# Kernel tuning notes

Hardware: AMD Instinct MI355X
Metric: run time of the kernel (lower is better)

Reference implementation:

```python
import jax, jax.numpy as jnp
import numpy as np

N = 50000   # n_nodes
F = 500     # n_features
D = 256     # architecture (GCN hidden)
K = 16      # n_clusters
E = 800000  # nnz of adjacency
CLUSTER_REG = 1.0
CON_REG = 0.5


def setup_inputs() -> dict:
    key = jax.random.key(0)
    ks = jax.random.split(key, 8)
    features = jax.random.normal(ks[0], (1, N, F), dtype=jnp.float32)
    aug_features = jax.random.normal(ks[1], (1, N, F), dtype=jnp.float32)
    graph_row = jax.random.randint(ks[2], (E,), 0, N, dtype=jnp.int32)
    graph_col = jax.random.randint(ks[3], (E,), 0, N, dtype=jnp.int32)
    graph_vals = jnp.ones((E,), jnp.float32)              # binary adjacency values
    gn_vals = jax.random.uniform(ks[4], (E,), jnp.float32)  # normalised adjacency values
    lbl = jnp.zeros((1, 2 * N), jnp.float32)              # unused in forward
    dense_graph = jnp.zeros((1,), jnp.float32)            # unused in forward
    # GCN params: Linear(F->D, bias=False) + separate zero bias (DGI-style GCN)
    W1 = jax.random.normal(ks[5], (D, F), dtype=jnp.float32) / np.sqrt(F)
    b1 = jnp.zeros((D,), jnp.float32)
    # transform: Linear(D->K) orthogonal-init weight, zero bias
    Wt = jax.random.normal(ks[6], (K, D), dtype=jnp.float32) / np.sqrt(D)
    bt = jnp.zeros((K,), jnp.float32)
    return {"features": features, "aug_features": aug_features,
            "graph_row": graph_row, "graph_col": graph_col,
            "graph_vals": graph_vals, "gn_vals": gn_vals,
            "lbl": lbl, "dense_graph": dense_graph,
            "W1": W1, "b1": b1, "Wt": Wt, "bt": bt}


def _spmm(row, col, vals, X):
    # (sparse NxN) @ X : out[i] = sum_j A[i,j] X[j]
    return jax.ops.segment_sum(vals[:, None] * X[col], row, num_segments=N)


def reference(features, aug_features, graph_row, graph_col, graph_vals, gn_vals,
              lbl, dense_graph, W1, b1, Wt, bt):
    def gcn(x):  # x: [1, N, F] -> [N, D]
        h = jnp.einsum('nf,df->nd', x[0], W1)      # Linear, no bias
        h = _spmm(graph_row, graph_col, gn_vals, h)  # A_norm @ h
        return jax.nn.selu(h + b1)

    gcn_out = gcn(features)                                  # [N, D]
    assignments = jax.nn.softmax(gcn_out @ Wt.T + bt, axis=1)  # [N, K]

    n_edges = jnp.float32(graph_vals.shape[0])
    degrees = jax.ops.segment_sum(graph_vals, graph_col, num_segments=N)[:, None]  # [N,1]

    AS = _spmm(graph_row, graph_col, graph_vals, assignments)  # A @ S, [N, K]
    graph_pooled = AS.T @ assignments                          # S^T A S, [K, K]
    nl = assignments.T @ degrees                               # [K, 1]
    normalizer = (nl @ nl.T) / 2.0 / n_edges                   # [K, K]
    spectral_loss = -jnp.trace(graph_pooled - normalizer) / 2.0 / n_edges

    cluster_sizes = assignments.sum(axis=0)                    # [K]
    cluster_loss = (jnp.linalg.norm(cluster_sizes) / N * np.sqrt(float(K)) - 1.0) * CLUSTER_REG

    aug_out = gcn(aug_features)                                # [N, D]
    # nn.CrossEntropyLoss(input=[1,N,D], target=[1,N,D] soft probs): class dim is N
    logsm = jax.nn.log_softmax(gcn_out, axis=0)                # softmax over nodes (dim=1 of [1,N,D])
    con_loss = -(aug_out * logsm).sum(axis=0).mean()

    return spectral_loss + cluster_loss + CON_REG * con_loss
```

## Files before the change

### kernel.cpp

```cpp
#include <hip/hip_runtime.h>
#include <math.h>

#define N_NODES 50000
#define N_FEAT  500
#define DH      256
#define KC      16
#define NE      800000
#define KPAD    512
#define MPAD    50048
#define M2      (2 * MPAD)
#define SLICE_COLS 32
#define NPAIR   8
#define SPMM_BLOCKS 2048
#define ROWS_PER_BLK 196
#define POST_BLOCKS 2048
#define SCAN_BLOCKS 196

#define R16(X) X(0) X(1) X(2) X(3) X(4) X(5) X(6) X(7) \
               X(8) X(9) X(10) X(11) X(12) X(13) X(14) X(15)

typedef __attribute__((ext_vector_type(8))) short short8;
typedef __attribute__((ext_vector_type(4))) float f32x4;

__device__ __forceinline__ unsigned short f2bf(float f) {
  unsigned u = __float_as_uint(f);
  u += 0x7FFFu + ((u >> 16) & 1u);
  return (unsigned short)(u >> 16);
}

__device__ __forceinline__ float bf2f(unsigned short u) {
  return __uint_as_float((unsigned)u << 16);
}

__device__ __forceinline__ float selu_f(float x) {
  return 1.0507009873554805f * (x > 0.f ? x : 1.6732632423543772f * expm1f(x));
}

__device__ __forceinline__ void gload16(const void* g, void* l) {
  __builtin_amdgcn_global_load_lds(
      (const __attribute__((address_space(1))) unsigned int*)g,
      (__attribute__((address_space(3))) unsigned int*)l, 16, 0, 0);
}

__global__ void k_cvt_w1(const float* __restrict__ in, unsigned short* __restrict__ out) {
  const int idx = blockIdx.x * 256 + threadIdx.x;
  if (idx >= DH * (KPAD / 8)) return;
  const int row = idx >> 6;
  const int cc  = idx & 63;
  const int scc = (cc & ~7) | ((cc & 7) ^ (row & 7));
  const int c0 = scc * 8;
  short8 w;
#pragma unroll
  for (int j = 0; j < 8; ++j) {
    const int col = c0 + j;
    w[j] = (col < N_FEAT) ? (short)f2bf(in[(size_t)row * N_FEAT + col]) : (short)0;
  }
  *(short8*)(out + (size_t)row * KPAD + cc * 8) = w;
}

__global__ __launch_bounds__(512, 2) void k_gemm_fused(
    const float* __restrict__ Af, const float* __restrict__ Aa,
    const unsigned short* __restrict__ Wbf, unsigned short* __restrict__ XWs) {
  __shared__ short As[128 * 64];
  __shared__ short Bs[256 * 64];
  const int t = threadIdx.x;
  const int lane = t & 63, wave = t >> 6;
  const int wr = (wave >> 2) * 64, wc = (wave & 3) * 64;
  const int bm = blockIdx.x * 128;
  const bool isaug = bm >= MPAD;
  const float* __restrict__ src = isaug ? Aa : Af;
  const int row0 = isaug ? bm - MPAD : bm;
  const int lr = lane & 15, lk = (lane >> 4) * 8;
  const int rsw = (lr & 7) * 8;
  const int ar = t >> 3, ac = (t & 7) * 8;
  const int aw = ac ^ ((ar & 7) * 8);
  f32x4 acc[4][4] = {};
  for (int kb = 0; kb < KPAD; kb += 64) {
    float4 ua[2][2];
#pragma unroll
    for (int h = 0; h < 2; ++h) {
      const int gr = row0 + ar + h * 64;
      const bool vr = gr < N_NODES;
      const float* arow = src + (size_t)(vr ? gr : 0) * N_FEAT;
      const int c = kb + ac;
      ua[h][0] = *(const float4*)(arow + min(c, N_FEAT - 4));
      ua[h][1] = *(const float4*)(arow + min(c + 4, N_FEAT - 4));
    }
#pragma unroll
    for (int i = 0; i < 4; ++i) {
      const int chunk = i * 512 + t;
      const int rb = chunk >> 3, sub = (chunk & 7) * 8;
      gload16(Wbf + (size_t)rb * KPAD + kb + sub, (void*)(Bs + (size_t)chunk * 8));
    }
#pragma unroll
    for (int h = 0; h < 2; ++h) {
      const int gr = row0 + ar + h * 64;
      const bool vr = gr < N_NODES;
      const int c = kb + ac;
      const bool ok0 = vr && (c < N_FEAT);
      const bool ok1 = vr && (c + 4 < N_FEAT);
      float4 u0 = ua[h][0], u1 = ua[h][1];
      u0.x = ok0 ? u0.x : 0.f; u0.y = ok0 ? u0.y : 0.f;
      u0.z = ok0 ? u0.z : 0.f; u0.w = ok0 ? u0.w : 0.f;
      u1.x = ok1 ? u1.x : 0.f; u1.y = ok1 ? u1.y : 0.f;
      u1.z = ok1 ? u1.z : 0.f; u1.w = ok1 ? u1.w : 0.f;
      short8 w;
      w[0] = (short)f2bf(u0.x); w[1] = (short)f2bf(u0.y);
      w[2] = (short)f2bf(u0.z); w[3] = (short)f2bf(u0.w);
      w[4] = (short)f2bf(u1.x); w[5] = (short)f2bf(u1.y);
      w[6] = (short)f2bf(u1.z); w[7] = (short)f2bf(u1.w);
      *(short8*)(As + (size_t)(ar + h * 64) * 64 + aw) = w;
    }
    __syncthreads();
#pragma unroll
    for (int kk = 0; kk < 64; kk += 32) {
      short8 af[4], bfr[4];
#pragma unroll
      for (int mi = 0; mi < 4; ++mi)
        af[mi] = *(const short8*)(As + (wr + mi * 16 + lr) * 64 + ((kk + lk) ^ rsw));
#pragma unroll
      for (int n = 0; n < 4; ++n)
        bfr[n] = *(const short8*)(Bs + (wc + n * 16 + lr) * 64 + ((kk + lk) ^ rsw));
#pragma unroll
      for (int mi = 0; mi < 4; ++mi)
#pragma unroll
        for (int n = 0; n < 4; ++n)
          acc[mi][n] = __builtin_amdgcn_mfma_f32_16x16x32_bf16(af[mi], bfr[n], acc[mi][n], 0, 0, 0);
    }
    __syncthreads();
  }
  const int crow = (lane >> 4) * 4, ccol = lane & 15;
  const int phb8 = isaug ? NPAIR : 0;
  const int snode = t >> 2, ssub = t & 3;
  const int csw = (snode & 7) * 8;
#pragma unroll
  for (int cb = 0; cb < 4; ++cb) {
    if ((wave & 3) == cb) {
#pragma unroll
      for (int mi = 0; mi < 4; ++mi)
#pragma unroll
        for (int n = 0; n < 4; ++n)
#pragma unroll
          for (int r = 0; r < 4; ++r)
            As[(wr + mi * 16 + crow + r) * 64 +
               ((n * 16 + ccol) ^ (((crow + r) & 7) * 8))] =
                (short)f2bf(acc[mi][n][r]);
    }
    __syncthreads();
#pragma unroll
    for (int p2 = 0; p2 < 2; ++p2) {
      const int pair = phb8 + cb * 2 + p2;
      const short8 vv = *(const short8*)(As + snode * 64 + ((p2 * 32 + ssub * 8) ^ csw));
      *(short8*)(XWs + ((size_t)pair * MPAD + row0 + snode) * SLICE_COLS + ssub * 8) = vv;
    }
    __syncthreads();
  }
}

__global__ void k_count(const int* __restrict__ row, int* __restrict__ counts) {
  const int e = blockIdx.x * blockDim.x + threadIdx.x;
  if (e < NE) atomicAdd(&counts[row[e]], 1);
}

__global__ __launch_bounds__(256) void k_scan_blk(const int* __restrict__ counts,
                                                  int* __restrict__ bsum) {
  __shared__ int red[256];
  const int t = threadIdx.x;
  const int j = blockIdx.x * 256 + t;
  red[t] = (j < N_NODES) ? counts[j] : 0;
  __syncthreads();
  for (int off = 128; off; off >>= 1) {
    if (t < off) red[t] += red[t + off];
    __syncthreads();
  }
  if (t == 0) bsum[blockIdx.x] = red[0];
}

__global__ __launch_bounds__(256) void k_scan_top(const int* __restrict__ bsum,
                                                  int* __restrict__ boff) {
  __shared__ int s[256];
  const int t = threadIdx.x;
  s[t] = (t < SCAN_BLOCKS) ? bsum[t] : 0;
  __syncthreads();
  for (int off = 1; off < 256; off <<= 1) {
    const int u = (t >= off) ? s[t - off] : 0;
    __syncthreads();
    s[t] += u;
    __syncthreads();
  }
  boff[t] = (t == 0) ? 0 : s[t - 1];
}

__global__ __launch_bounds__(256) void k_scan_fin(const int* __restrict__ counts,
                                                  const int* __restrict__ boff,
                                                  int* __restrict__ row_ptr,
                                                  int* __restrict__ cursor) {
  __shared__ int s[256];
  const int t = threadIdx.x;
  const int j = blockIdx.x * 256 + t;
  const int v = (j < N_NODES) ? counts[j] : 0;
  s[t] = v;
  __syncthreads();
  for (int off = 1; off < 256; off <<= 1) {
    const int u = (t >= off) ? s[t - off] : 0;
    __syncthreads();
    s[t] += u;
    __syncthreads();
  }
  const int excl = boff[blockIdx.x] + s[t] - v;
  if (j < N_NODES) { row_ptr[j] = excl; cursor[j] = excl; }
  if (j == N_NODES - 1) row_ptr[N_NODES] = excl + v;
}

__global__ void k_scatter(const int* __restrict__ row, const int* __restrict__ col,
                          const float* __restrict__ gnv, int* __restrict__ cursor,
                          int* __restrict__ ecol, float* __restrict__ eval) {
  const int e = blockIdx.x * blockDim.x + threadIdx.x;
  if (e < NE) {
    const int p = atomicAdd(&cursor[row[e]], 1);
    ecol[p] = col[e];
    eval[p] = gnv[e];
  }
}

__global__ __launch_bounds__(256, 4) void k_spmm_slice(
    const int* __restrict__ row_ptr, const int* __restrict__ ecol, const float* __restrict__ eval,
    const unsigned short* __restrict__ XWp,
    const float* __restrict__ b1,
    unsigned short* __restrict__ Ob) {
  const int slice = blockIdx.x & 7;
  const int rblk  = blockIdx.x >> 3;
  const int r0 = rblk * ROWS_PER_BLK;
  const int r1 = min(r0 + ROWS_PER_BLK, N_NODES);
  const int wave = threadIdx.x >> 6, lane = threadIdx.x & 63;
  const int g = lane >> 2, sub = lane & 3;
  const int scol = slice * SLICE_COLS + sub * 8;

  const float4 b0 = *(const float4*)(b1 + scol);
  const float4 b4 = *(const float4*)(b1 + scol + 4);
  const unsigned short* __restrict__ Xb =
      XWp + (size_t)slice * MPAD * SLICE_COLS + sub * 8;

  for (int rb = r0; rb < r1; rb += 64) {
    const int row = rb + wave * 16 + g;
    if (row >= r1) continue;
    const int s = row_ptr[row], e = row_ptr[row + 1];
    float acc[8] = {0.f, 0.f, 0.f, 0.f, 0.f, 0.f, 0.f, 0.f};
    int p = s;
    for (; p + 1 < e; p += 2) {
      const int   c0 = ecol[p],  c1 = ecol[p + 1];
      const float v0 = eval[p],  v1 = eval[p + 1];
      const short8 x0 = *(const short8*)(Xb + (size_t)c0 * SLICE_COLS);
      const short8 x1 = *(const short8*)(Xb + (size_t)c1 * SLICE_COLS);
#pragma unroll
      for (int u = 0; u < 8; ++u) {
        acc[u] += v0 * bf2f((unsigned short)x0[u]);
        acc[u] += v1 * bf2f((unsigned short)x1[u]);
      }
    }
    if (p < e) {
      const int   c0 = ecol[p];
      const float v0 = eval[p];
      const short8 x0 = *(const short8*)(Xb + (size_t)c0 * SLICE_COLS);
#pragma unroll
      for (int u = 0; u < 8; ++u) acc[u] += v0 * bf2f((unsigned short)x0[u]);
    }
    short8 o;
    o[0] = (short)f2bf(selu_f(acc[0] + b0.x));
    o[1] = (short)f2bf(selu_f(acc[1] + b0.y));
    o[2] = (short)f2bf(selu_f(acc[2] + b0.z));
    o[3] = (short)f2bf(selu_f(acc[3] + b0.w));
    o[4] = (short)f2bf(selu_f(acc[4] + b4.x));
    o[5] = (short)f2bf(selu_f(acc[5] + b4.y));
    o[6] = (short)f2bf(selu_f(acc[6] + b4.z));
    o[7] = (short)f2bf(selu_f(acc[7] + b4.w));
    *(short8*)(Ob + (size_t)row * DH + scol) = o;
  }
}

__global__ __launch_bounds__(256, 2) void k_post(
    const unsigned short* __restrict__ O, const float* __restrict__ Wt,
    const float* __restrict__ bt, float* __restrict__ S,
    float* __restrict__ exptot, float* __restrict__ augtot,
    float* __restrict__ csg, float* __restrict__ dotAG) {
  __shared__ float expacc[DH];
  __shared__ float augacc[DH];
  __shared__ float csacc[KC];
  __shared__ float dacc;
  expacc[threadIdx.x] = 0.f;
  augacc[threadIdx.x] = 0.f;
  if (threadIdx.x < KC) csacc[threadIdx.x] = 0.f;
  if (threadIdx.x == 0) dacc = 0.f;
  __syncthreads();

  const int wave = threadIdx.x >> 6, lane = threadIdx.x & 63;
  const int c0 = lane * 4;
  const unsigned short* Of = O;
  const unsigned short* Oa = O + (size_t)N_NODES * DH;

  float lexp0 = 0.f, lexp1 = 0.f, lexp2 = 0.f, lexp3 = 0.f;
  float laug0 = 0.f, laug1 = 0.f, laug2 = 0.f, laug3 = 0.f;
  float ldot = 0.f, lcs = 0.f;
#define LDBT(K) const float bt_##K = bt[K];
  R16(LDBT)
#undef LDBT

  for (int i = blockIdx.x * 4 + wave; i < N_NODES; i += POST_BLOCKS * 4) {
    const ushort4 fu = *(const ushort4*)(Of + (size_t)i * DH + c0);
    const ushort4 au = *(const ushort4*)(Oa + (size_t)i * DH + c0);
    const float of0 = bf2f(fu.x), of1 = bf2f(fu.y), of2 = bf2f(fu.z), of3 = bf2f(fu.w);
    const float oa0 = bf2f(au.x), oa1 = bf2f(au.y), oa2 = bf2f(au.z), oa3 = bf2f(au.w);
    lexp0 += expf(of0); lexp1 += expf(of1); lexp2 += expf(of2); lexp3 += expf(of3);
    laug0 += oa0; laug1 += oa1; laug2 += oa2; laug3 += oa3;
    ldot += of0 * oa0 + of1 * oa1 + of2 * oa2 + of3 * oa3;

#define DOT(K) float l##K; { const float4 w = *(const float4*)(Wt + K * DH + c0); \
                             l##K = of0 * w.x + of1 * w.y + of2 * w.z + of3 * w.w; }
    R16(DOT)
#undef DOT
#pragma unroll
    for (int off = 32; off; off >>= 1) {
#define SHF(K) l##K += __shfl_xor(l##K, off);
      R16(SHF)
#undef SHF
    }
#define BIAS(K) l##K += bt_##K;
    R16(BIAS)
#undef BIAS
    float mx = l0;
#define MX(K) mx = fmaxf(mx, l##K);
    R16(MX)
#undef MX
    float se = 0.f;
#define EXPK(K) l##K = expf(l##K - mx); se += l##K;
    R16(EXPK)
#undef EXPK
    const float inv = 1.f / se;
    float myv = 0.f;
#define SEL(K) if (lane == K) myv = l##K;
    R16(SEL)
#undef SEL
    if (lane < KC) {
      const float sv = myv * inv;
      S[(size_t)i * KC + lane] = sv;
      lcs += sv;
    }
  }

#pragma unroll
  for (int off = 32; off; off >>= 1) ldot += __shfl_xor(ldot, off);
  if (lane == 0) atomicAdd(&dacc, ldot);
  atomicAdd(&expacc[c0 + 0], lexp0);
  atomicAdd(&expacc[c0 + 1], lexp1);
  atomicAdd(&expacc[c0 + 2], lexp2);
  atomicAdd(&expacc[c0 + 3], lexp3);
  atomicAdd(&augacc[c0 + 0], laug0);
  atomicAdd(&augacc[c0 + 1], laug1);
  atomicAdd(&augacc[c0 + 2], laug2);
  atomicAdd(&augacc[c0 + 3], laug3);
  if (lane < KC) atomicAdd(&csacc[lane], lcs);
  __syncthreads();
  atomicAdd(&exptot[threadIdx.x], expacc[threadIdx.x]);
  atomicAdd(&augtot[threadIdx.x], augacc[threadIdx.x]);
  if (threadIdx.x < KC) atomicAdd(&csg[threadIdx.x], csacc[threadIdx.x]);
  if (threadIdx.x == 0) atomicAdd(dotAG, dacc);
}

__global__ __launch_bounds__(256) void k_edge(const int* __restrict__ grow, const int* __restrict__ gcol,
                                              const float* __restrict__ gvals, const float* __restrict__ S,
                                              float* __restrict__ nl, float* __restrict__ tp) {
  float ltp = 0.f;
  float lnl[KC];
#pragma unroll
  for (int k = 0; k < KC; ++k) lnl[k] = 0.f;
  for (long e = (long)blockIdx.x * 256 + threadIdx.x; e < NE; e += (long)gridDim.x * 256) {
    const int r = grow[e], c = gcol[e];
    const float v = gvals[e];
    const float4* sr = (const float4*)(S + (size_t)r * KC);
    const float4* sc = (const float4*)(S + (size_t)c * KC);
    const float4 a0 = sr[0], a1 = sr[1], a2 = sr[2], a3 = sr[3];
    const float4 b0 = sc[0], b1v = sc[1], b2 = sc[2], b3 = sc[3];
    const float dot = a0.x * b0.x + a0.y * b0.y + a0.z * b0.z + a0.w * b0.w
                    + a1.x * b1v.x + a1.y * b1v.y + a1.z * b1v.z + a1.w * b1v.w
                    + a2.x * b2.x + a2.y * b2.y + a2.z * b2.z + a2.w * b2.w
                    + a3.x * b3.x + a3.y * b3.y + a3.z * b3.z + a3.w * b3.w;
    ltp += v * dot;
    lnl[0] += v * b0.x;  lnl[1] += v * b0.y;  lnl[2] += v * b0.z;  lnl[3] += v * b0.w;
    lnl[4] += v * b1v.x; lnl[5] += v * b1v.y; lnl[6] += v * b1v.z; lnl[7] += v * b1v.w;
    lnl[8] += v * b2.x;  lnl[9] += v * b2.y;  lnl[10] += v * b2.z; lnl[11] += v * b2.w;
    lnl[12] += v * b3.x; lnl[13] += v * b3.y; lnl[14] += v * b3.z; lnl[15] += v * b3.w;
  }
#pragma unroll
  for (int off = 32; off; off >>= 1) {
    ltp += __shfl_xor(ltp, off);
#pragma unroll
    for (int k = 0; k < KC; ++k) lnl[k] += __shfl_xor(lnl[k], off);
  }
  __shared__ float wred[4][KC + 1];
  const int wave = threadIdx.x >> 6, lane = threadIdx.x & 63;
  if (lane == 0) {
    wred[wave][0] = ltp;
#pragma unroll
    for (int k = 0; k < KC; ++k) wred[wave][1 + k] = lnl[k];
  }
  __syncthreads();
  if (threadIdx.x < KC + 1) {
    const float s = wred[0][threadIdx.x] + wred[1][threadIdx.x] + wred[2][threadIdx.x] + wred[3][threadIdx.x];
    if (threadIdx.x == 0) atomicAdd(tp, s);
    else atomicAdd(&nl[threadIdx.x - 1], s);
  }
}

__global__ void k_final(const float* __restrict__ exptot, const float* __restrict__ augtot,
                        const float* __restrict__ scal, float* __restrict__ out) {
  const int d = threadIdx.x;
  const float L = logf(exptot[d]);
  const float sa = augtot[d];
  __shared__ float red[DH];
  red[d] = L * sa;
  __syncthreads();
  for (int off = 128; off; off >>= 1) {
    if (d < off) red[d] += red[d + off];
    __syncthreads();
  }
  if (d == 0) {
    const float sumLA = red[0];
    const float dotAG = scal[0];
    const float tp = scal[1];
    float nl2 = 0.f, cs2 = 0.f;
#pragma unroll
    for (int k = 0; k < KC; ++k) {
      nl2 += scal[2 + k] * scal[2 + k];
      cs2 += scal[18 + k] * scal[18 + k];
    }
    const float fE = (float)NE;
    const float con = -(dotAG - sumLA) / (float)DH;
    const float trn = nl2 / (2.f * fE);
    const float spectral = -(tp - trn) / (2.f * fE);
    const float cluster = (sqrtf(cs2) / (float)N_NODES * 4.f - 1.f);
    out[0] = spectral + cluster + 0.5f * con;
  }
}

extern "C" void kernel_launch(void* const* d_in, const int* in_sizes, int n_in,
                              void* d_out, int out_size, void* d_ws, size_t ws_size,
                              hipStream_t stream) {
  const float* features = (const float*)d_in[0];
  const float* augf     = (const float*)d_in[1];
  const int*   grow     = (const int*)d_in[2];
  const int*   gcol     = (const int*)d_in[3];
  const float* gvals    = (const float*)d_in[4];
  const float* gnv      = (const float*)d_in[5];
  const float* W1       = (const float*)d_in[8];
  const float* b1       = (const float*)d_in[9];
  const float* Wt       = (const float*)d_in[10];
  const float* bt       = (const float*)d_in[11];

  char* ws = (char*)d_ws;
  size_t off = 0;
  auto alloc = [&](size_t bytes) -> void* {
    void* p = ws + off;
    off = (off + bytes + 255) & ~(size_t)255;
    return p;
  };
  unsigned short* Wbf  = (unsigned short*)alloc((size_t)DH * KPAD * 2);
  unsigned short* XWs  = (unsigned short*)alloc((size_t)16 * MPAD * SLICE_COLS * 2);
  unsigned short* O    = (unsigned short*)alloc((size_t)2 * N_NODES * DH * 2);
  float* S       = (float*)alloc((size_t)N_NODES * KC * 4);
  int*   ecol    = (int*)alloc((size_t)NE * 4);
  float* eval    = (float*)alloc((size_t)NE * 4);
  int*   row_ptr = (int*)alloc((size_t)(N_NODES + 1) * 4);
  int*   cursor  = (int*)alloc((size_t)N_NODES * 4);
  int*   counts  = (int*)alloc((size_t)N_NODES * 4);
  int*   bsum    = (int*)alloc((size_t)256 * 4);
  int*   boff    = (int*)alloc((size_t)256 * 4);
  float* exptot  = (float*)alloc((size_t)DH * 4);
  float* augtot  = (float*)alloc((size_t)DH * 4);
  float* scal    = (float*)alloc(64 * 4);
  if (off > ws_size) return;

  hipMemsetAsync(counts, 0, (size_t)N_NODES * 4, stream);
  hipMemsetAsync(exptot, 0, (size_t)DH * 4 * 2 + 64 * 4, stream);

  k_cvt_w1<<<64, 256, 0, stream>>>(W1, Wbf);

  k_count<<<(NE + 255) / 256, 256, 0, stream>>>(grow, counts);
  k_scan_blk<<<SCAN_BLOCKS, 256, 0, stream>>>(counts, bsum);
  k_scan_top<<<1, 256, 0, stream>>>(bsum, boff);
  k_scan_fin<<<SCAN_BLOCKS, 256, 0, stream>>>(counts, boff, row_ptr, cursor);
  k_scatter<<<(NE + 255) / 256, 256, 0, stream>>>(grow, gcol, gnv, cursor, ecol, eval);

  k_gemm_fused<<<M2 / 128, 512, 0, stream>>>(features, augf, Wbf, XWs);

  k_spmm_slice<<<SPMM_BLOCKS, 256, 0, stream>>>(row_ptr, ecol, eval,
                                                XWs, b1, O);
  k_spmm_slice<<<SPMM_BLOCKS, 256, 0, stream>>>(row_ptr, ecol, eval,
                                                XWs + (size_t)NPAIR * MPAD * SLICE_COLS,
                                                b1, O + (size_t)N_NODES * DH);

  k_post<<<POST_BLOCKS, 256, 0, stream>>>(O, Wt, bt, S, exptot, augtot,
                                          scal + 18, scal + 0);

  k_edge<<<512, 256, 0, stream>>>(grow, gcol, gvals, S, scal + 2, scal + 1);

  k_final<<<1, 256, 0, stream>>>(exptot, augtot, scal, (float*)d_out);
}
```

Baseline: 488.7 us.

## Prefetch GEMM A tiles across iterations, raise occupancy, pack edge col/val

The fused GEMM now loads the next k-block of fp32 features into registers right after the LDS barrier, so those global loads overlap the MFMA work on the current tile. It also loads A fragments one at a time to reduce register pressure and raises the launch-bounds occupancy hint from 2 to 4 blocks per CU. Separately, the CSR column indices and values are packed into one int2 array, so each SpMM edge costs a single 8-byte load instead of two scattered 4-byte loads. The higher occupancy target may force register spills in the GEMM.

```diff
diff --git a/kernel.cpp b/kernel.cpp
--- a/kernel.cpp
+++ b/kernel.cpp
@@ -58,7 +58,7 @@
   *(short8*)(out + (size_t)row * KPAD + cc * 8) = w;
 }
 
-__global__ __launch_bounds__(512, 2) void k_gemm_fused(
+__global__ __launch_bounds__(512, 4) void k_gemm_fused(
     const float* __restrict__ Af, const float* __restrict__ Aa,
     const unsigned short* __restrict__ Wbf, unsigned short* __restrict__ XWs) {
   __shared__ short As[128 * 64];
@@ -74,18 +74,19 @@
   const int rsw = (lr & 7) * 8;
   const int ar = t >> 3, ac = (t & 7) * 8;
   const int aw = ac ^ ((ar & 7) * 8);
+  const int gr0 = row0 + ar, gr1 = row0 + ar + 64;
+  const float* const arow0 = src + (size_t)(gr0 < N_NODES ? gr0 : 0) * N_FEAT;
+  const float* const arow1 = src + (size_t)(gr1 < N_NODES ? gr1 : 0) * N_FEAT;
   f32x4 acc[4][4] = {};
+  float4 ua[2][2];
+  {
+    const int c = ac;
+    ua[0][0] = *(const float4*)(arow0 + min(c, N_FEAT - 4));
+    ua[0][1] = *(const float4*)(arow0 + min(c + 4, N_FEAT - 4));
+    ua[1][0] = *(const float4*)(arow1 + min(c, N_FEAT - 4));
+    ua[1][1] = *(const float4*)(arow1 + min(c + 4, N_FEAT - 4));
+  }
   for (int kb = 0; kb < KPAD; kb += 64) {
-    float4 ua[2][2];
-#pragma unroll
-    for (int h = 0; h < 2; ++h) {
-      const int gr = row0 + ar + h * 64;
-      const bool vr = gr < N_NODES;
-      const float* arow = src + (size_t)(vr ? gr : 0) * N_FEAT;
-      const int c = kb + ac;
-      ua[h][0] = *(const float4*)(arow + min(c, N_FEAT - 4));
-      ua[h][1] = *(const float4*)(arow + min(c + 4, N_FEAT - 4));
-    }
 #pragma unroll
     for (int i = 0; i < 4; ++i) {
       const int chunk = i * 512 + t;
@@ -94,7 +95,7 @@
     }
 #pragma unroll
     for (int h = 0; h < 2; ++h) {
-      const int gr = row0 + ar + h * 64;
+      const int gr = h ? gr1 : gr0;
       const bool vr = gr < N_NODES;
       const int c = kb + ac;
       const bool ok0 = vr && (c < N_FEAT);
@@ -112,20 +113,26 @@
       *(short8*)(As + (size_t)(ar + h * 64) * 64 + aw) = w;
     }
     __syncthreads();
+    if (kb + 64 < KPAD) {
+      const int c = kb + 64 + ac;
+      ua[0][0] = *(const float4*)(arow0 + min(c, N_FEAT - 4));
+      ua[0][1] = *(const float4*)(arow0 + min(c + 4, N_FEAT - 4));
+      ua[1][0] = *(const float4*)(arow1 + min(c, N_FEAT - 4));
+      ua[1][1] = *(const float4*)(arow1 + min(c + 4, N_FEAT - 4));
+    }
 #pragma unroll
     for (int kk = 0; kk < 64; kk += 32) {
-      short8 af[4], bfr[4];
-#pragma unroll
-      for (int mi = 0; mi < 4; ++mi)
-        af[mi] = *(const short8*)(As + (wr + mi * 16 + lr) * 64 + ((kk + lk) ^ rsw));
+      short8 bfr[4];
 #pragma unroll
       for (int n = 0; n < 4; ++n)
         bfr[n] = *(const short8*)(Bs + (wc + n * 16 + lr) * 64 + ((kk + lk) ^ rsw));
 #pragma unroll
-      for (int mi = 0; mi < 4; ++mi)
+      for (int mi = 0; mi < 4; ++mi) {
+        const short8 a = *(const short8*)(As + (wr + mi * 16 + lr) * 64 + ((kk + lk) ^ rsw));
 #pragma unroll
         for (int n = 0; n < 4; ++n)
-          acc[mi][n] = __builtin_amdgcn_mfma_f32_16x16x32_bf16(af[mi], bfr[n], acc[mi][n], 0, 0, 0);
+          acc[mi][n] = __builtin_amdgcn_mfma_f32_16x16x32_bf16(a, bfr[n], acc[mi][n], 0, 0, 0);
+      }
     }
     __syncthreads();
   }
@@ -214,17 +221,16 @@
 
 __global__ void k_scatter(const int* __restrict__ row, const int* __restrict__ col,
                           const float* __restrict__ gnv, int* __restrict__ cursor,
-                          int* __restrict__ ecol, float* __restrict__ eval) {
+                          int2* __restrict__ epack) {
   const int e = blockIdx.x * blockDim.x + threadIdx.x;
   if (e < NE) {
     const int p = atomicAdd(&cursor[row[e]], 1);
-    ecol[p] = col[e];
-    eval[p] = gnv[e];
+    epack[p] = make_int2(col[e], __float_as_int(gnv[e]));
   }
 }
 
 __global__ __launch_bounds__(256, 4) void k_spmm_slice(
-    const int* __restrict__ row_ptr, const int* __restrict__ ecol, const float* __restrict__ eval,
+    const int* __restrict__ row_ptr, const int2* __restrict__ epack,
     const unsigned short* __restrict__ XWp,
     const float* __restrict__ b1,
     unsigned short* __restrict__ Ob) {
@@ -248,10 +254,10 @@
     float acc[8] = {0.f, 0.f, 0.f, 0.f, 0.f, 0.f, 0.f, 0.f};
     int p = s;
     for (; p + 1 < e; p += 2) {
-      const int   c0 = ecol[p],  c1 = ecol[p + 1];
-      const float v0 = eval[p],  v1 = eval[p + 1];
-      const short8 x0 = *(const short8*)(Xb + (size_t)c0 * SLICE_COLS);
-      const short8 x1 = *(const short8*)(Xb + (size_t)c1 * SLICE_COLS);
+      const int2 e0 = epack[p], e1 = epack[p + 1];
+      const float v0 = __int_as_float(e0.y), v1 = __int_as_float(e1.y);
+      const short8 x0 = *(const short8*)(Xb + (size_t)e0.x * SLICE_COLS);
+      const short8 x1 = *(const short8*)(Xb + (size_t)e1.x * SLICE_COLS);
 #pragma unroll
       for (int u = 0; u < 8; ++u) {
         acc[u] += v0 * bf2f((unsigned short)x0[u]);
@@ -259,9 +265,9 @@
       }
     }
     if (p < e) {
-      const int   c0 = ecol[p];
-      const float v0 = eval[p];
-      const short8 x0 = *(const short8*)(Xb + (size_t)c0 * SLICE_COLS);
+      const int2 e0 = epack[p];
+      const float v0 = __int_as_float(e0.y);
+      const short8 x0 = *(const short8*)(Xb + (size_t)e0.x * SLICE_COLS);
 #pragma unroll
       for (int u = 0; u < 8; ++u) acc[u] += v0 * bf2f((unsigned short)x0[u]);
     }
@@ -467,8 +473,7 @@
   unsigned short* XWs  = (unsigned short*)alloc((size_t)16 * MPAD * SLICE_COLS * 2);
   unsigned short* O    = (unsigned short*)alloc((size_t)2 * N_NODES * DH * 2);
   float* S       = (float*)alloc((size_t)N_NODES * KC * 4);
-  int*   ecol    = (int*)alloc((size_t)NE * 4);
-  float* eval    = (float*)alloc((size_t)NE * 4);
+  int2*  epack   = (int2*)alloc((size_t)NE * 8);
   int*   row_ptr = (int*)alloc((size_t)(N_NODES + 1) * 4);
   int*   cursor  = (int*)alloc((size_t)N_NODES * 4);
   int*   counts  = (int*)alloc((size_t)N_NODES * 4);
@@ -488,13 +493,13 @@
   k_scan_blk<<<SCAN_BLOCKS, 256, 0, stream>>>(counts, bsum);
   k_scan_top<<<1, 256, 0, stream>>>(bsum, boff);
   k_scan_fin<<<SCAN_BLOCKS, 256, 0, stream>>>(counts, boff, row_ptr, cursor);
-  k_scatter<<<(NE + 255) / 256, 256, 0, stream>>>(grow, gcol, gnv, cursor, ecol, eval);
+  k_scatter<<<(NE + 255) / 256, 256, 0, stream>>>(grow, gcol, gnv, cursor, epack);
 
   k_gemm_fused<<<M2 / 128, 512, 0, stream>>>(features, augf, Wbf, XWs);
 
-  k_spmm_slice<<<SPMM_BLOCKS, 256, 0, stream>>>(row_ptr, ecol, eval,
+  k_spmm_slice<<<SPMM_BLOCKS, 256, 0, stream>>>(row_ptr, epack,
                                                 XWs, b1, O);
-  k_spmm_slice<<<SPMM_BLOCKS, 256, 0, stream>>>(row_ptr, ecol, eval,
+  k_spmm_slice<<<SPMM_BLOCKS, 256, 0, stream>>>(row_ptr, epack,
                                                 XWs + (size_t)NPAIR * MPAD * SLICE_COLS,
                                                 b1, O + (size_t)N_NODES * DH);
 
```

New measurement: 444.8 us. 9.0% less time.
